# Kernel optimization log

Measured on AMD Instinct MI355X. Metric: run time of the kernel, lower is better.

## Reference

```python
import jax, jax.numpy as jnp
import numpy as np

B, S, HID = 1, 2048, 2048
HQ, HKV, D = 32, 8, 64
GROUPS = HQ // HKV
SCALE = 1.0 / np.sqrt(D)
GN_EPS = 1e-5


def rotate_half(x):
    x1, x2 = jnp.split(x, 2, axis=-1)
    return jnp.concatenate([-x2, x1], axis=-1)


def apply_rope(x, cos, sin):
    # x: [B,S,H,D]; cos/sin: [S,D] broadcast over batch and heads
    c = cos[None, :, None, :]
    s = sin[None, :, None, :]
    return x * c + rotate_half(x) * s


def setup_inputs() -> dict:
    key = jax.random.key(0)
    ks = jax.random.split(key, 8)
    w = 0.02
    x = jax.random.normal(ks[0], (B, S, HID), dtype=jnp.float32)
    # standard RoPE tables
    inv_freq = 1.0 / (10000.0 ** (np.arange(0, D, 2, dtype=np.float32) / D))
    freqs = np.arange(S, dtype=np.float32)[:, None] * inv_freq[None, :]  # [S, D/2]
    emb = np.concatenate([freqs, freqs], axis=-1)  # [S, D]
    rope_cos = jnp.asarray(np.cos(emb), dtype=jnp.float32)
    rope_sin = jnp.asarray(np.sin(emb), dtype=jnp.float32)
    Wq = jax.random.normal(ks[1], (HID, HQ * D), dtype=jnp.float32) * w
    Wk = jax.random.normal(ks[2], (HID, HKV * D), dtype=jnp.float32) * w
    Wv = jax.random.normal(ks[3], (HID, HKV * D), dtype=jnp.float32) * w
    Wo = jax.random.normal(ks[4], (HQ * D, HID), dtype=jnp.float32) * w
    Wg = jax.random.normal(ks[5], (HID, HQ * D), dtype=jnp.float32) * w
    bg = jnp.zeros((HQ * D,), dtype=jnp.float32)
    gn_weight = jnp.ones((HQ * D,), dtype=jnp.float32)
    gn_bias = jnp.zeros((HQ * D,), dtype=jnp.float32)
    return {"x": x, "rope_cos": rope_cos, "rope_sin": rope_sin, "Wq": Wq, "Wk": Wk,
            "Wv": Wv, "Wo": Wo, "Wg": Wg, "bg": bg, "gn_weight": gn_weight,
            "gn_bias": gn_bias}


def reference(x, rope_cos, rope_sin, Wq, Wk, Wv, Wo, Wg, bg, gn_weight, gn_bias):
    # projections
    q = (x @ Wq).reshape(B, S, HQ, D)
    k = (x @ Wk).reshape(B, S, HKV, D)
    v = (x @ Wv).reshape(B, S, HKV, D)
    q = apply_rope(q, rope_cos, rope_sin)
    k = apply_rope(k, rope_cos, rope_sin)
    # to [B, H, S, D]
    q = q.transpose(0, 2, 1, 3)
    k = k.transpose(0, 2, 1, 3)
    v = v.transpose(0, 2, 1, 3)
    new_k, new_v = k, v  # kv_cache output (pre GQA-expansion)
    # GQA expand kv heads: repeat_interleave along head axis
    k_e = jnp.repeat(k, GROUPS, axis=1)
    v_e = jnp.repeat(v, GROUPS, axis=1)
    # scores [B, HQ, S, S]
    attn = jnp.einsum('bhqd,bhkd->bhqk', q, k_e) * SCALE
    # causal mask (S_k == S, no cache)
    row = jnp.arange(S)[:, None]
    col = jnp.arange(S)[None, :]
    attn = jnp.where(col > row, -jnp.inf, attn)
    # manual softmax as in source: exp(a - max) / (sum + 1e-9), nan_to_num
    m = jnp.max(attn, axis=-1, keepdims=True)
    p = jnp.exp(attn - m)
    p = p / (jnp.sum(p, axis=-1, keepdims=True) + 1e-9)
    p = jnp.nan_to_num(p, nan=0.0)
    out = jnp.einsum('bhqk,bhkd->bhqd', p, v_e)  # [B,HQ,S,D]
    out = out.transpose(0, 2, 1, 3)  # [B,S,HQ,D]
    # GroupNorm(num_groups=HQ) on channels HQ*D per token => per-head norm over D
    mu = jnp.mean(out, axis=-1, keepdims=True)
    var = jnp.mean(jnp.square(out - mu), axis=-1, keepdims=True)
    gn = (out - mu) / jnp.sqrt(var + GN_EPS)
    gn = gn * gn_weight.reshape(HQ, D) + gn_bias.reshape(HQ, D)
    gn = gn.reshape(B, S, HQ * D)
    # sigmoid gate + output projection
    alpha = jax.nn.sigmoid(x @ Wg + bg)
    y = (gn * alpha) @ Wo
    return (y, new_k, new_v)
```

## Files before the change

### kernel.cpp

```cpp
#include <hip/hip_runtime.h>
#include <hip/hip_bf16.h>
#include <stdint.h>

#define S_LEN 2048
#define HID_DIM 2048
#define HQ 32
#define HKV 8
#define NPROJ 5120
#define QSCALE_LOG2 (0.125f * 1.44269504088896f)

using f32x4 = __attribute__((ext_vector_type(4))) float;
using bfrag = __attribute__((ext_vector_type(8))) short;

__device__ __forceinline__ unsigned short f2bf(float f) {
    union { float f; unsigned u; } a; a.f = f;
    unsigned r = a.u + 0x7fffu + ((a.u >> 16) & 1u);
    return (unsigned short)(r >> 16);
}
__device__ __forceinline__ float bf2f(unsigned short h) {
    union { unsigned u; float f; } a; a.u = ((unsigned)h) << 16;
    return a.f;
}

__device__ __forceinline__ void gload16(const void* g, void* l) {
    __builtin_amdgcn_global_load_lds((const __attribute__((address_space(1))) unsigned int*)g,
                                     (__attribute__((address_space(3))) unsigned int*)l, 16, 0, 0);
}

__global__ void k_convert_x(const float* __restrict__ x, unsigned short* __restrict__ xb, int n4) {
    int i = blockIdx.x * blockDim.x + threadIdx.x;
    if (i < n4) {
        float4 v = ((const float4*)x)[i];
        ushort4 o;
        o.x = f2bf(v.x); o.y = f2bf(v.y); o.z = f2bf(v.z); o.w = f2bf(v.w);
        ((ushort4*)xb)[i] = o;
    }
}

__global__ void k_transpose_w(const float* __restrict__ src, unsigned short* __restrict__ dst,
                              int K, int N, int rowOff) {
    __shared__ float tile[32][33];
    int n0 = blockIdx.x * 32;
    int k0 = blockIdx.y * 32;
    int lx = threadIdx.x & 31;
    int ly = threadIdx.x >> 5;
#pragma unroll
    for (int i = 0; i < 4; i++) {
        int r = ly + i * 8;
        tile[r][lx] = src[(size_t)(k0 + r) * N + n0 + lx];
    }
    __syncthreads();
#pragma unroll
    for (int i = 0; i < 4; i++) {
        int nn = ly + i * 8;
        dst[(size_t)(rowOff + n0 + nn) * K + k0 + lx] = f2bf(tile[lx][nn]);
    }
}

__global__ __launch_bounds__(256) void k_gemm_bf16(
        const unsigned short* __restrict__ A,
        const unsigned short* __restrict__ Bt,
        float* __restrict__ C,
        int M, int N, int K) {
    __shared__ __align__(16) unsigned short As[128 * 64];
    __shared__ __align__(16) unsigned short Bs[128 * 64];
    const int tid = threadIdx.x;
    const int lane = tid & 63;
    const int w = tid >> 6;
    const int wm = (w >> 1) * 64, wn = (w & 1) * 64;
    const int bm0 = blockIdx.y * 128, bn0 = blockIdx.x * 128;
    const int lr = lane & 15;
    const int lk = (lane >> 4) * 8;
    const int srow_in = lane >> 3;
    const int scol = (lane & 7) * 8;

    f32x4 acc[4][4] = {};

    for (int k0 = 0; k0 < K; k0 += 64) {
        __syncthreads();
#pragma unroll
        for (int p = 0; p < 4; p++) {
            int chunk = p * 4 + w;
            int row = chunk * 8 + srow_in;
            gload16(&A[(size_t)(bm0 + row) * K + k0 + scol], &As[chunk * 512]);
            gload16(&Bt[(size_t)(bn0 + row) * K + k0 + scol], &Bs[chunk * 512]);
        }
        __syncthreads();
#pragma unroll
        for (int kc = 0; kc < 2; kc++) {
            bfrag af[4], bfr[4];
#pragma unroll
            for (int t = 0; t < 4; t++)
                af[t] = *(const bfrag*)&As[(wm + t * 16 + lr) * 64 + kc * 32 + lk];
#pragma unroll
            for (int t = 0; t < 4; t++)
                bfr[t] = *(const bfrag*)&Bs[(wn + t * 16 + lr) * 64 + kc * 32 + lk];
#pragma unroll
            for (int mt = 0; mt < 4; mt++)
#pragma unroll
                for (int nt = 0; nt < 4; nt++)
                    acc[mt][nt] = __builtin_amdgcn_mfma_f32_16x16x32_bf16(af[mt], bfr[nt], acc[mt][nt], 0, 0, 0);
        }
    }
    const int orow = (lane >> 4) * 4;
#pragma unroll
    for (int mt = 0; mt < 4; mt++)
#pragma unroll
        for (int nt = 0; nt < 4; nt++)
#pragma unroll
            for (int j = 0; j < 4; j++)
                C[(size_t)(bm0 + wm + mt * 16 + orow + j) * N + bn0 + wn + nt * 16 + lr] = acc[mt][nt][j];
}

__global__ void k_epilogue(const float* __restrict__ proj,
                           const float* __restrict__ cosb, const float* __restrict__ sinb,
                           const float* __restrict__ bg,
                           unsigned short* __restrict__ qb,
                           unsigned short* __restrict__ kbuf,
                           unsigned short* __restrict__ vt,
                           unsigned short* __restrict__ alpha,
                           float* __restrict__ outk, float* __restrict__ outv) {
    int idx = blockIdx.x * 256 + threadIdx.x;
    int s = idx / NPROJ;
    int n = idx - s * NPROJ;
    float val = proj[idx];
    if (n < 2048) {
        int h = n >> 6, d = n & 63;
        float c = cosb[(s << 6) + d], sn = sinb[(s << 6) + d];
        float partner = proj[(size_t)s * NPROJ + (d < 32 ? n + 32 : n - 32)];
        float rot = (d < 32) ? -partner : partner;
        float o = val * c + rot * sn;
        qb[((size_t)h * S_LEN + s) * 64 + d] = f2bf(o * QSCALE_LOG2);
    } else if (n < 2560) {
        int m = n - 2048;
        int h = m >> 6, d = m & 63;
        float c = cosb[(s << 6) + d], sn = sinb[(s << 6) + d];
        float partner = proj[(size_t)s * NPROJ + (d < 32 ? n + 32 : n - 32)];
        float rot = (d < 32) ? -partner : partner;
        float o = val * c + rot * sn;
        size_t oidx = ((size_t)h * S_LEN + s) * 64 + d;
        kbuf[oidx] = f2bf(o);
        outk[oidx] = o;
    } else if (n < 3072) {
        int m = n - 2560;
        int h = m >> 6, d = m & 63;
        vt[((size_t)h * 64 + d) * S_LEN + s] = f2bf(val);
        outv[((size_t)h * S_LEN + s) * 64 + d] = val;
    } else {
        int m = n - 3072;
        float a = 1.0f / (1.0f + __expf(-(val + bg[m])));
        alpha[(size_t)s * 2048 + m] = f2bf(a);
    }
}

__global__ __launch_bounds__(256) void k_attn(
        const unsigned short* __restrict__ qb,
        const unsigned short* __restrict__ kbuf,
        const unsigned short* __restrict__ vt,
        float* __restrict__ ao) {
    __shared__ __align__(16) unsigned short Ks[2][64 * 64];
    __shared__ __align__(16) unsigned short Vs[2][64 * 64];
    __shared__ __align__(16) unsigned short Ps[4][16 * 72];
    const int tid = threadIdx.x;
    const int lane = tid & 63;
    const int w = tid >> 6;
    const int lr = lane & 15;
    const int lg = lane >> 4;
    const int lk = lg * 8;

    const int bid = blockIdx.x;
    const int qblk = 31 - (bid >> 5);
    const int h = bid & 31;
    const int hk = h >> 2;
    const int r0 = qblk * 64 + w * 16;

    const int swzkey = (lr & 7) << 4;
    const int swz0 = ((lg * 16) ^ swzkey) >> 1;
    const int swz1 = ((64 + lg * 16) ^ swzkey) >> 1;
    const int srow = lane >> 3;
    const int scol = (((lane & 7) ^ srow) << 3);

    const unsigned short* Kg = &kbuf[(size_t)hk * S_LEN * 64];
    const unsigned short* Vg = &vt[(size_t)hk * 64 * S_LEN];

    bfrag qf[2];
    {
        const unsigned short* qrow = &qb[((size_t)h * S_LEN + r0 + lr) * 64];
        qf[0] = *(const bfrag*)&qrow[lk];
        qf[1] = *(const bfrag*)&qrow[32 + lk];
    }

    float m_r[4], l_r[4];
    f32x4 o_acc[4] = {};
#pragma unroll
    for (int j = 0; j < 4; j++) { m_r[j] = -1e30f; l_r[j] = 0.0f; }

#define STAGE(buf, kb)                                                                  \
    {                                                                                   \
        _Pragma("unroll")                                                               \
        for (int c = 0; c < 2; c++) {                                                   \
            int chunk = w * 2 + c;                                                      \
            gload16(&Kg[(size_t)((kb) * 64 + chunk * 8 + srow) * 64 + scol],            \
                    &Ks[buf][chunk * 512]);                                             \
            gload16(&Vg[(size_t)(chunk * 8 + srow) * S_LEN + (kb) * 64 + scol],         \
                    &Vs[buf][chunk * 512]);                                             \
        }                                                                               \
    }

    const int nt = qblk + 1;
    STAGE(0, 0);
    __syncthreads();
    int cur = 0;

    for (int kb = 0; kb < nt; kb++) {
        if (kb + 1 < nt) STAGE(cur ^ 1, kb + 1);
        const unsigned short* Kc = Ks[cur];
        const unsigned short* Vc = Vs[cur];
        f32x4 sacc[4] = {};
        __builtin_amdgcn_s_setprio(1);
#pragma unroll
        for (int g = 0; g < 4; g++) {
            bfrag kf0 = *(const bfrag*)&Kc[g * 1024 + lr * 64 + swz0];
            bfrag kf1 = *(const bfrag*)&Kc[g * 1024 + lr * 64 + swz1];
            sacc[g] = __builtin_amdgcn_mfma_f32_16x16x32_bf16(qf[0], kf0, sacc[g], 0, 0, 0);
            sacc[g] = __builtin_amdgcn_mfma_f32_16x16x32_bf16(qf[1], kf1, sacc[g], 0, 0, 0);
        }
        __builtin_amdgcn_s_setprio(0);
        if (kb == qblk) {
#pragma unroll
            for (int g = 0; g < 4; g++)
#pragma unroll
                for (int j = 0; j < 4; j++) {
                    int col = kb * 64 + g * 16 + lr;
                    int row = r0 + lg * 4 + j;
                    if (col > row) sacc[g][j] = -1e30f;
                }
        }
        float ps[4];
#pragma unroll
        for (int j = 0; j < 4; j++) {
            float tv = fmaxf(fmaxf(sacc[0][j], sacc[1][j]), fmaxf(sacc[2][j], sacc[3][j]));
#pragma unroll
            for (int msk = 1; msk < 16; msk <<= 1)
                tv = fmaxf(tv, __shfl_xor(tv, msk, 64));
            float mnew = fmaxf(m_r[j], tv);
            float sc = exp2f(m_r[j] - mnew);
            m_r[j] = mnew;
            l_r[j] *= sc;
#pragma unroll
            for (int g = 0; g < 4; g++) o_acc[g][j] *= sc;
            ps[j] = 0.0f;
        }
#pragma unroll
        for (int g = 0; g < 4; g++)
#pragma unroll
            for (int j = 0; j < 4; j++) {
                float p = exp2f(sacc[g][j] - m_r[j]);
                ps[j] += p;
                Ps[w][(lg * 4 + j) * 72 + g * 16 + lr] = f2bf(p);
            }
#pragma unroll
        for (int j = 0; j < 4; j++) {
            float pv = ps[j];
#pragma unroll
            for (int msk = 1; msk < 16; msk <<= 1)
                pv += __shfl_xor(pv, msk, 64);
            l_r[j] += pv;
        }
        bfrag pf0 = *(const bfrag*)&Ps[w][lr * 72 + lk];
        bfrag pf1 = *(const bfrag*)&Ps[w][lr * 72 + 32 + lk];
        __builtin_amdgcn_s_setprio(1);
#pragma unroll
        for (int g = 0; g < 4; g++) {
            bfrag vf0 = *(const bfrag*)&Vc[g * 1024 + lr * 64 + swz0];
            bfrag vf1 = *(const bfrag*)&Vc[g * 1024 + lr * 64 + swz1];
            o_acc[g] = __builtin_amdgcn_mfma_f32_16x16x32_bf16(pf0, vf0, o_acc[g], 0, 0, 0);
            o_acc[g] = __builtin_amdgcn_mfma_f32_16x16x32_bf16(pf1, vf1, o_acc[g], 0, 0, 0);
        }
        __builtin_amdgcn_s_setprio(0);
        __syncthreads();
        cur ^= 1;
    }
#undef STAGE

    float inv[4];
#pragma unroll
    for (int j = 0; j < 4; j++) inv[j] = 1.0f / (l_r[j] + 1e-9f);
#pragma unroll
    for (int g = 0; g < 4; g++)
#pragma unroll
        for (int j = 0; j < 4; j++) {
            int row = r0 + lg * 4 + j;
            ao[((size_t)h * S_LEN + row) * 64 + g * 16 + lr] = o_acc[g][j] * inv[j];
        }
}

__global__ void k_gn(const float* __restrict__ ao, const unsigned short* __restrict__ alpha,
                     const float* __restrict__ gnw, const float* __restrict__ gnb,
                     unsigned short* __restrict__ gno) {
    int row = blockIdx.x * 4 + (threadIdx.x >> 6);
    int d = threadIdx.x & 63;
    int h = row >> 11;
    int s = row & 2047;
    float v = ao[(size_t)row * 64 + d];
    float mu = v;
#pragma unroll
    for (int msk = 1; msk < 64; msk <<= 1) mu += __shfl_xor(mu, msk, 64);
    mu *= (1.0f / 64.0f);
    float dv = v - mu;
    float var = dv * dv;
#pragma unroll
    for (int msk = 1; msk < 64; msk <<= 1) var += __shfl_xor(var, msk, 64);
    var *= (1.0f / 64.0f);
    int col = (h << 6) + d;
    float g = dv * rsqrtf(var + 1e-5f) * gnw[col] + gnb[col];
    float a = bf2f(alpha[(size_t)s * 2048 + col]);
    gno[(size_t)s * 2048 + col] = f2bf(g * a);
}

extern "C" void kernel_launch(void* const* d_in, const int* in_sizes, int n_in,
                              void* d_out, int out_size, void* d_ws, size_t ws_size,
                              hipStream_t stream) {
    const float* x   = (const float*)d_in[0];
    const float* rc  = (const float*)d_in[1];
    const float* rs  = (const float*)d_in[2];
    const float* Wq  = (const float*)d_in[3];
    const float* Wk  = (const float*)d_in[4];
    const float* Wv  = (const float*)d_in[5];
    const float* Wo  = (const float*)d_in[6];
    const float* Wg  = (const float*)d_in[7];
    const float* bg  = (const float*)d_in[8];
    const float* gnw = (const float*)d_in[9];
    const float* gnb = (const float*)d_in[10];
    float* out = (float*)d_out;

    char* ws = (char*)d_ws;
    unsigned short* xb    = (unsigned short*)(ws);
    unsigned short* WcatT = (unsigned short*)(ws + 8388608);
    unsigned short* WoT   = (unsigned short*)(ws + 29360128);
    float*          proj  = (float*)(ws + 37748736);
    unsigned short* alpha = (unsigned short*)(ws + 8388608);
    unsigned short* qb    = (unsigned short*)(ws + 16777216);
    unsigned short* kbuf  = (unsigned short*)(ws + 25165824);
    unsigned short* vt    = (unsigned short*)(ws + 27262976);
    float*          ao    = (float*)(ws + 37748736);
    unsigned short* gno   = (unsigned short*)(ws + 54525952);

    hipLaunchKernelGGL(k_convert_x, dim3(4096), dim3(256), 0, stream, x, xb, 2048 * 2048 / 4);
    hipLaunchKernelGGL(k_transpose_w, dim3(64, 64), dim3(256), 0, stream, Wq, WcatT, 2048, 2048, 0);
    hipLaunchKernelGGL(k_transpose_w, dim3(16, 64), dim3(256), 0, stream, Wk, WcatT, 2048, 512, 2048);
    hipLaunchKernelGGL(k_transpose_w, dim3(16, 64), dim3(256), 0, stream, Wv, WcatT, 2048, 512, 2560);
    hipLaunchKernelGGL(k_transpose_w, dim3(64, 64), dim3(256), 0, stream, Wg, WcatT, 2048, 2048, 3072);
    hipLaunchKernelGGL(k_transpose_w, dim3(64, 64), dim3(256), 0, stream, Wo, WoT, 2048, 2048, 0);

    hipLaunchKernelGGL(k_gemm_bf16, dim3(5120 / 128, 2048 / 128), dim3(256), 0, stream,
                       xb, WcatT, proj, 2048, 5120, 2048);

    float* outk = out + (size_t)4 * 1024 * 1024;
    float* outv = out + (size_t)5 * 1024 * 1024;
    hipLaunchKernelGGL(k_epilogue, dim3(2048 * 5120 / 256), dim3(256), 0, stream,
                       proj, rc, rs, bg, qb, kbuf, vt, alpha, outk, outv);

    hipLaunchKernelGGL(k_attn, dim3(1024), dim3(256), 0, stream, qb, kbuf, vt, ao);

    hipLaunchKernelGGL(k_gn, dim3(32 * 2048 / 4), dim3(256), 0, stream, ao, alpha, gnw, gnb, gno);

    hipLaunchKernelGGL(k_gemm_bf16, dim3(2048 / 128, 2048 / 128), dim3(256), 0, stream,
                       gno, WoT, out, 2048, 2048, 2048);
}
```

Before: 376.7 us.

## Fuse RoPE/sigmoid epilogue into projection GEMM and GroupNorm into attention

Replaces the separate fp32 projection buffer and elementwise epilogue kernel with a dedicated projection GEMM. Its register epilogue applies RoPE (using the accumulator tile 32 columns away as the rotate-half partner), writes V transposed, and computes the sigmoid gate. It also folds the per-head GroupNorm and gating into the end of the attention kernel using 16-lane shuffles, removing the fp32 attention-output round trip and two launches. The cost is a heavier GEMM epilogue with scattered, partly uncoalesced stores (vt writes strided by S) and more register pressure in the attention tail.

```diff
diff --git a/kernel.cpp b/kernel.cpp
--- a/kernel.cpp
+++ b/kernel.cpp
@@ -112,44 +112,118 @@
                 C[(size_t)(bm0 + wm + mt * 16 + orow + j) * N + bn0 + wn + nt * 16 + lr] = acc[mt][nt][j];
 }
 
-__global__ void k_epilogue(const float* __restrict__ proj,
-                           const float* __restrict__ cosb, const float* __restrict__ sinb,
-                           const float* __restrict__ bg,
-                           unsigned short* __restrict__ qb,
-                           unsigned short* __restrict__ kbuf,
-                           unsigned short* __restrict__ vt,
-                           unsigned short* __restrict__ alpha,
-                           float* __restrict__ outk, float* __restrict__ outv) {
-    int idx = blockIdx.x * 256 + threadIdx.x;
-    int s = idx / NPROJ;
-    int n = idx - s * NPROJ;
-    float val = proj[idx];
-    if (n < 2048) {
-        int h = n >> 6, d = n & 63;
-        float c = cosb[(s << 6) + d], sn = sinb[(s << 6) + d];
-        float partner = proj[(size_t)s * NPROJ + (d < 32 ? n + 32 : n - 32)];
-        float rot = (d < 32) ? -partner : partner;
-        float o = val * c + rot * sn;
-        qb[((size_t)h * S_LEN + s) * 64 + d] = f2bf(o * QSCALE_LOG2);
-    } else if (n < 2560) {
-        int m = n - 2048;
-        int h = m >> 6, d = m & 63;
-        float c = cosb[(s << 6) + d], sn = sinb[(s << 6) + d];
-        float partner = proj[(size_t)s * NPROJ + (d < 32 ? n + 32 : n - 32)];
-        float rot = (d < 32) ? -partner : partner;
-        float o = val * c + rot * sn;
-        size_t oidx = ((size_t)h * S_LEN + s) * 64 + d;
-        kbuf[oidx] = f2bf(o);
-        outk[oidx] = o;
-    } else if (n < 3072) {
-        int m = n - 2560;
-        int h = m >> 6, d = m & 63;
-        vt[((size_t)h * 64 + d) * S_LEN + s] = f2bf(val);
-        outv[((size_t)h * S_LEN + s) * 64 + d] = val;
+__global__ __launch_bounds__(256) void k_gemm_proj(
+        const unsigned short* __restrict__ A,
+        const unsigned short* __restrict__ Bt,
+        const float* __restrict__ rc, const float* __restrict__ rs,
+        const float* __restrict__ bg,
+        unsigned short* __restrict__ qb,
+        unsigned short* __restrict__ kbuf,
+        unsigned short* __restrict__ vt,
+        unsigned short* __restrict__ alpha,
+        float* __restrict__ outk, float* __restrict__ outv) {
+    __shared__ __align__(16) unsigned short As[128 * 64];
+    __shared__ __align__(16) unsigned short Bs[128 * 64];
+    const int tid = threadIdx.x;
+    const int lane = tid & 63;
+    const int w = tid >> 6;
+    const int wm = (w >> 1) * 64, wn = (w & 1) * 64;
+    const int bcol = blockIdx.x;
+    const int bm0 = blockIdx.y * 128, bn0 = bcol * 128;
+    const int lr = lane & 15;
+    const int lk = (lane >> 4) * 8;
+    const int srow_in = lane >> 3;
+    const int scol = (lane & 7) * 8;
+    const int K = HID_DIM;
+
+    f32x4 acc[4][4] = {};
+
+    for (int k0 = 0; k0 < K; k0 += 64) {
+        __syncthreads();
+#pragma unroll
+        for (int p = 0; p < 4; p++) {
+            int chunk = p * 4 + w;
+            int row = chunk * 8 + srow_in;
+            gload16(&A[(size_t)(bm0 + row) * K + k0 + scol], &As[chunk * 512]);
+            gload16(&Bt[(size_t)(bn0 + row) * K + k0 + scol], &Bs[chunk * 512]);
+        }
+        __syncthreads();
+#pragma unroll
+        for (int kc = 0; kc < 2; kc++) {
+            bfrag af[4], bfr[4];
+#pragma unroll
+            for (int t = 0; t < 4; t++)
+                af[t] = *(const bfrag*)&As[(wm + t * 16 + lr) * 64 + kc * 32 + lk];
+#pragma unroll
+            for (int t = 0; t < 4; t++)
+                bfr[t] = *(const bfrag*)&Bs[(wn + t * 16 + lr) * 64 + kc * 32 + lk];
+#pragma unroll
+            for (int mt = 0; mt < 4; mt++)
+#pragma unroll
+                for (int nt = 0; nt < 4; nt++)
+                    acc[mt][nt] = __builtin_amdgcn_mfma_f32_16x16x32_bf16(af[mt], bfr[nt], acc[mt][nt], 0, 0, 0);
+        }
+    }
+
+    const int orow = (lane >> 4) * 4;
+    if (bcol < 20) {
+        const bool isq = (bcol < 16);
+#pragma unroll
+        for (int mt = 0; mt < 4; mt++)
+#pragma unroll
+            for (int j = 0; j < 4; j++) {
+                const int s = bm0 + wm + mt * 16 + orow + j;
+#pragma unroll
+                for (int nt = 0; nt < 4; nt++) {
+                    const int n = bn0 + wn + nt * 16 + lr;
+                    const int d = n & 63;
+                    const float c = rc[(s << 6) + d];
+                    const float sn = rs[(s << 6) + d];
+                    const float val = acc[mt][nt][j];
+                    const float partner = acc[mt][nt ^ 2][j];
+                    const float rot = (nt < 2) ? -partner : partner;
+                    const float o = val * c + rot * sn;
+                    if (isq) {
+                        const int h = n >> 6;
+                        qb[((size_t)h * S_LEN + s) * 64 + d] = f2bf(o * QSCALE_LOG2);
+                    } else {
+                        const int h = (n - 2048) >> 6;
+                        const size_t oidx = ((size_t)h * S_LEN + s) * 64 + d;
+                        kbuf[oidx] = f2bf(o);
+                        outk[oidx] = o;
+                    }
+                }
+            }
+    } else if (bcol < 24) {
+#pragma unroll
+        for (int mt = 0; mt < 4; mt++)
+#pragma unroll
+            for (int j = 0; j < 4; j++) {
+                const int s = bm0 + wm + mt * 16 + orow + j;
+#pragma unroll
+                for (int nt = 0; nt < 4; nt++) {
+                    const int n = bn0 + wn + nt * 16 + lr;
+                    const int h = (n - 2560) >> 6;
+                    const int d = n & 63;
+                    const float val = acc[mt][nt][j];
+                    vt[((size_t)h * 64 + d) * S_LEN + s] = f2bf(val);
+                    outv[((size_t)h * S_LEN + s) * 64 + d] = val;
+                }
+            }
     } else {
-        int m = n - 3072;
-        float a = 1.0f / (1.0f + __expf(-(val + bg[m])));
-        alpha[(size_t)s * 2048 + m] = f2bf(a);
+#pragma unroll
+        for (int mt = 0; mt < 4; mt++)
+#pragma unroll
+            for (int j = 0; j < 4; j++) {
+                const int s = bm0 + wm + mt * 16 + orow + j;
+#pragma unroll
+                for (int nt = 0; nt < 4; nt++) {
+                    const int n = bn0 + wn + nt * 16 + lr;
+                    const int m = n - 3072;
+                    const float a = 1.0f / (1.0f + __expf(-(acc[mt][nt][j] + bg[m])));
+                    alpha[(size_t)s * 2048 + m] = f2bf(a);
+                }
+            }
     }
 }
 
@@ -157,7 +231,9 @@
         const unsigned short* __restrict__ qb,
         const unsigned short* __restrict__ kbuf,
         const unsigned short* __restrict__ vt,
-        float* __restrict__ ao) {
+        const unsigned short* __restrict__ alpha,
+        const float* __restrict__ gnw, const float* __restrict__ gnb,
+        unsigned short* __restrict__ gno) {
     __shared__ __align__(16) unsigned short Ks[2][64 * 64];
     __shared__ __align__(16) unsigned short Vs[2][64 * 64];
     __shared__ __align__(16) unsigned short Ps[4][16 * 72];
@@ -283,39 +359,34 @@
     }
 #undef STAGE
 
-    float inv[4];
-#pragma unroll
-    for (int j = 0; j < 4; j++) inv[j] = 1.0f / (l_r[j] + 1e-9f);
-#pragma unroll
-    for (int g = 0; g < 4; g++)
-#pragma unroll
-        for (int j = 0; j < 4; j++) {
-            int row = r0 + lg * 4 + j;
-            ao[((size_t)h * S_LEN + row) * 64 + g * 16 + lr] = o_acc[g][j] * inv[j];
-        }
-}
-
-__global__ void k_gn(const float* __restrict__ ao, const unsigned short* __restrict__ alpha,
-                     const float* __restrict__ gnw, const float* __restrict__ gnb,
-                     unsigned short* __restrict__ gno) {
-    int row = blockIdx.x * 4 + (threadIdx.x >> 6);
-    int d = threadIdx.x & 63;
-    int h = row >> 11;
-    int s = row & 2047;
-    float v = ao[(size_t)row * 64 + d];
-    float mu = v;
-#pragma unroll
-    for (int msk = 1; msk < 64; msk <<= 1) mu += __shfl_xor(mu, msk, 64);
-    mu *= (1.0f / 64.0f);
-    float dv = v - mu;
-    float var = dv * dv;
-#pragma unroll
-    for (int msk = 1; msk < 64; msk <<= 1) var += __shfl_xor(var, msk, 64);
-    var *= (1.0f / 64.0f);
-    int col = (h << 6) + d;
-    float g = dv * rsqrtf(var + 1e-5f) * gnw[col] + gnb[col];
-    float a = bf2f(alpha[(size_t)s * 2048 + col]);
-    gno[(size_t)s * 2048 + col] = f2bf(g * a);
+    float gv[4][4];
+#pragma unroll
+    for (int j = 0; j < 4; j++) {
+        const float inv = 1.0f / (l_r[j] + 1e-9f);
+#pragma unroll
+        for (int g = 0; g < 4; g++) gv[g][j] = o_acc[g][j] * inv;
+    }
+#pragma unroll
+    for (int j = 0; j < 4; j++) {
+        float sum = gv[0][j] + gv[1][j] + gv[2][j] + gv[3][j];
+#pragma unroll
+        for (int msk = 1; msk < 16; msk <<= 1) sum += __shfl_xor(sum, msk, 64);
+        const float mu = sum * (1.0f / 64.0f);
+        float vs = 0.0f;
+#pragma unroll
+        for (int g = 0; g < 4; g++) { float dd = gv[g][j] - mu; vs += dd * dd; }
+#pragma unroll
+        for (int msk = 1; msk < 16; msk <<= 1) vs += __shfl_xor(vs, msk, 64);
+        const float rstd = rsqrtf(vs * (1.0f / 64.0f) + 1e-5f);
+        const int s = r0 + lg * 4 + j;
+#pragma unroll
+        for (int g = 0; g < 4; g++) {
+            const int col = (h << 6) + g * 16 + lr;
+            const float gn = (gv[g][j] - mu) * rstd * gnw[col] + gnb[col];
+            const float a = bf2f(alpha[(size_t)s * 2048 + col]);
+            gno[(size_t)s * 2048 + col] = f2bf(gn * a);
+        }
+    }
 }
 
 extern "C" void kernel_launch(void* const* d_in, const int* in_sizes, int n_in,
@@ -338,13 +409,11 @@
     unsigned short* xb    = (unsigned short*)(ws);
     unsigned short* WcatT = (unsigned short*)(ws + 8388608);
     unsigned short* WoT   = (unsigned short*)(ws + 29360128);
-    float*          proj  = (float*)(ws + 37748736);
-    unsigned short* alpha = (unsigned short*)(ws + 8388608);
-    unsigned short* qb    = (unsigned short*)(ws + 16777216);
-    unsigned short* kbuf  = (unsigned short*)(ws + 25165824);
-    unsigned short* vt    = (unsigned short*)(ws + 27262976);
-    float*          ao    = (float*)(ws + 37748736);
-    unsigned short* gno   = (unsigned short*)(ws + 54525952);
+    unsigned short* alpha = (unsigned short*)(ws + 37748736);
+    unsigned short* qb    = (unsigned short*)(ws + 46137344);
+    unsigned short* kbuf  = (unsigned short*)(ws + 54525952);
+    unsigned short* vt    = (unsigned short*)(ws + 56623104);
+    unsigned short* gno   = (unsigned short*)(ws + 58720256);
 
     hipLaunchKernelGGL(k_convert_x, dim3(4096), dim3(256), 0, stream, x, xb, 2048 * 2048 / 4);
     hipLaunchKernelGGL(k_transpose_w, dim3(64, 64), dim3(256), 0, stream, Wq, WcatT, 2048, 2048, 0);
@@ -353,17 +422,14 @@
     hipLaunchKernelGGL(k_transpose_w, dim3(64, 64), dim3(256), 0, stream, Wg, WcatT, 2048, 2048, 3072);
     hipLaunchKernelGGL(k_transpose_w, dim3(64, 64), dim3(256), 0, stream, Wo, WoT, 2048, 2048, 0);
 
-    hipLaunchKernelGGL(k_gemm_bf16, dim3(5120 / 128, 2048 / 128), dim3(256), 0, stream,
-                       xb, WcatT, proj, 2048, 5120, 2048);
-
     float* outk = out + (size_t)4 * 1024 * 1024;
     float* outv = out + (size_t)5 * 1024 * 1024;
-    hipLaunchKernelGGL(k_epilogue, dim3(2048 * 5120 / 256), dim3(256), 0, stream,
-                       proj, rc, rs, bg, qb, kbuf, vt, alpha, outk, outv);
-
-    hipLaunchKernelGGL(k_attn, dim3(1024), dim3(256), 0, stream, qb, kbuf, vt, ao);
-
-    hipLaunchKernelGGL(k_gn, dim3(32 * 2048 / 4), dim3(256), 0, stream, ao, alpha, gnw, gnb, gno);
+
+    hipLaunchKernelGGL(k_gemm_proj, dim3(5120 / 128, 2048 / 128), dim3(256), 0, stream,
+                       xb, WcatT, rc, rs, bg, qb, kbuf, vt, alpha, outk, outv);
+
+    hipLaunchKernelGGL(k_attn, dim3(1024), dim3(256), 0, stream,
+                       qb, kbuf, vt, alpha, gnw, gnb, gno);
 
     hipLaunchKernelGGL(k_gemm_bf16, dim3(2048 / 128, 2048 / 128), dim3(256), 0, stream,
                        gno, WoT, out, 2048, 2048, 2048);
```

Result: slower. 405.6 us (+7.7%).
